# Optimization experiments

Hardware: AMD Instinct MI355X
Metric: run time of the kernel (lower is better)

Reference implementation:

```python
import jax, jax.numpy as jnp
import numpy as np

D_MODEL = 512
NUM_HEADS = 8
D_K = D_MODEL // NUM_HEADS


def setup_inputs() -> dict:
    key = jax.random.key(0)
    kx, kq, kk, kv, ko = jax.random.split(key, 5)
    scale = 1.0 / np.sqrt(D_MODEL)
    return {
        "x": jax.random.normal(kx, (2, 4096, D_MODEL), dtype=jnp.float32),
        "Wq": jax.random.normal(kq, (D_MODEL, D_MODEL), dtype=jnp.float32) * scale,
        "Wk": jax.random.normal(kk, (D_MODEL, D_MODEL), dtype=jnp.float32) * scale,
        "Wv": jax.random.normal(kv, (D_MODEL, D_MODEL), dtype=jnp.float32) * scale,
        "Wo": jax.random.normal(ko, (D_MODEL, D_MODEL), dtype=jnp.float32) * scale,
    }


def reference(x, Wq, Wk, Wv, Wo):
    B, T, D = x.shape
    H, dk = NUM_HEADS, D_K
    # Linear(d,d, bias=False): y = x @ W.T ; weights stored [out,in] like torch
    q = (x @ Wq.T).reshape(B, T, H, dk).transpose(0, 2, 1, 3)  # [B,H,T,dk]
    k = (x @ Wk.T).reshape(B, T, H, dk).transpose(0, 2, 1, 3)
    v = (x @ Wv.T).reshape(B, T, H, dk).transpose(0, 2, 1, 3)
    scores = jnp.einsum("bhqd,bhkd->bhqk", q, k) / np.sqrt(dk)  # [B,H,T,T]
    probs = jax.nn.softmax(scores, axis=-1)
    o = jnp.einsum("bhqk,bhkd->bhqd", probs, v)  # [B,H,T,dk]
    o = o.transpose(0, 2, 1, 3).reshape(B, T, D)
    return o @ Wo.T
```

## Files before the change

### kernel.cpp

```cpp
#include <hip/hip_runtime.h>
#include <hip/hip_bf16.h>

#define SEQ 4096
#define DMODEL 512
#define HEADS 8
#define DK 64
#define BATCH 2
#define MTOT (BATCH * SEQ)
#define NBH (BATCH * HEADS)

typedef __attribute__((ext_vector_type(8))) short bh8;
typedef __attribute__((ext_vector_type(4))) float f4;
typedef __attribute__((ext_vector_type(16))) float f16x;
typedef __attribute__((ext_vector_type(2))) float f2;

union uf { f16x v; f2 h[8]; };

#define MFMA(a, b, c)   __builtin_amdgcn_mfma_f32_16x16x32_bf16(a, b, c, 0, 0, 0)
#define MFMA32(a, b, c) __builtin_amdgcn_mfma_f32_32x32x16_bf16(a, b, c, 0, 0, 0)
#define GLL16(g, l) __builtin_amdgcn_global_load_lds( \
    (const __attribute__((address_space(1))) void*)(g), \
    (__attribute__((address_space(3))) void*)(l), 16, 0, 0)

__device__ __forceinline__ unsigned short f2b(float f) {
    union { float f; unsigned u; } v; v.f = f;
    unsigned r = v.u + 0x7fff + ((v.u >> 16) & 1);
    return (unsigned short)(r >> 16);
}

__device__ __forceinline__ unsigned cvtpk(float lo, float hi) {
    unsigned r;
    asm("v_cvt_pk_bf16_f32 %0, %1, %2" : "=v"(r) : "v"(lo), "v"(hi));
    return r;
}
__device__ __forceinline__ void plswap(unsigned& a, unsigned& b) {
    asm("v_permlane32_swap_b32 %0, %1" : "+v"(a), "+v"(b));
}
__device__ __forceinline__ float wave_max_pair(float x) {
    float b = x; asm("" : "+v"(b));
    float a = x;
    asm("v_permlane32_swap_b32 %0, %1" : "+v"(a), "+v"(b));
    return fmaxf(a, b);
}
__device__ __forceinline__ float wave_sum_pair(float x) {
    float b = x; asm("" : "+v"(b));
    float a = x;
    asm("v_permlane32_swap_b32 %0, %1" : "+v"(a), "+v"(b));
    return a + b;
}
__device__ __forceinline__ f2 pk_add(f2 a, f2 b) {
    f2 d; asm("v_pk_add_f32 %0, %1, %2" : "=v"(d) : "v"(a), "v"(b)); return d;
}
__device__ __forceinline__ f2 pk_mul(f2 a, f2 b) {
    f2 d; asm("v_pk_mul_f32 %0, %1, %2" : "=v"(d) : "v"(a), "v"(b)); return d;
}
__device__ __forceinline__ float max3f(float a, float b, float c) {
    float d; asm("v_max3_f32 %0, %1, %2, %3" : "=v"(d) : "v"(a), "v"(b), "v"(c));
    return d;
}

__global__ __launch_bounds__(256) void convert_k(
    const float* __restrict__ x, const float* __restrict__ wq,
    const float* __restrict__ wk, const float* __restrict__ wv,
    const float* __restrict__ wo, unsigned short* __restrict__ dst)
{
    const size_t i = ((size_t)blockIdx.x * 256 + threadIdx.x) * 4;
    const float* s; size_t o;
    if (i < 4194304u)                 { s = x;  o = i; }
    else if (i < 4194304u + 262144u)  { s = wq; o = i - 4194304u; }
    else if (i < 4194304u + 524288u)  { s = wk; o = i - (4194304u + 262144u); }
    else if (i < 4194304u + 786432u)  { s = wv; o = i - (4194304u + 524288u); }
    else                              { s = wo; o = i - (4194304u + 786432u); }
    float4 v = *(const float4*)(s + o);
    ushort4 u; u.x = f2b(v.x); u.y = f2b(v.y); u.z = f2b(v.z); u.w = f2b(v.w);
    *(ushort4*)(dst + i) = u;
}

__global__ __launch_bounds__(256) void qkv_gemm_mfma(
    const unsigned short* __restrict__ xb,
    const unsigned short* __restrict__ Wb,
    unsigned short* __restrict__ QKV)
{
    const int z = blockIdx.z;
    const unsigned short* A = xb;
    const unsigned short* B = Wb + (size_t)z * (DMODEL * DMODEL);
    const int m0 = blockIdx.x * 128, n0 = blockIdx.y * 128;
    const int tid = threadIdx.x, w = tid >> 6, l = tid & 63;
    const int wr = w >> 1, wc = w & 1;

    __shared__ __align__(16) unsigned short As[128 * 32];
    __shared__ __align__(16) unsigned short Bs[128 * 32];

    f4 acc[4][4] = {};
    const int lrow = l >> 2, lslot = l & 3;

    for (int k0 = 0; k0 < DMODEL; k0 += 32) {
        __syncthreads();
        #pragma unroll
        for (int j = 0; j < 2; ++j) {
            const int row = w * 32 + j * 16 + lrow;
            const int sw = lslot ^ ((row >> 1) & 3);
            GLL16(A + (size_t)(m0 + row) * DMODEL + k0 + sw * 8,
                  (char*)As + (w * 32 + j * 16) * 64);
            GLL16(B + (size_t)(n0 + row) * DMODEL + k0 + sw * 8,
                  (char*)Bs + (w * 32 + j * 16) * 64);
        }
        __syncthreads();
        bh8 af[4], bg[4];
        #pragma unroll
        for (int mi = 0; mi < 4; ++mi) {
            const int r = wr * 64 + mi * 16 + (l & 15);
            af[mi] = *(const bh8*)((const char*)As + r * 64 +
                                   (((l >> 4) * 16) ^ (((r >> 1) & 3) << 4)));
        }
        #pragma unroll
        for (int ni = 0; ni < 4; ++ni) {
            const int r = wc * 64 + ni * 16 + (l & 15);
            bg[ni] = *(const bh8*)((const char*)Bs + r * 64 +
                                   (((l >> 4) * 16) ^ (((r >> 1) & 3) << 4)));
        }
        #pragma unroll
        for (int mi = 0; mi < 4; ++mi)
            #pragma unroll
            for (int ni = 0; ni < 4; ++ni)
                acc[mi][ni] = MFMA(af[mi], bg[ni], acc[mi][ni]);
    }

    unsigned short* Out = QKV + (size_t)z * ((size_t)NBH * SEQ * DK);
    const float sc = (z == 0) ? 0.18033688011112042f : 1.0f;
    #pragma unroll
    for (int mi = 0; mi < 4; ++mi) {
        #pragma unroll
        for (int rg = 0; rg < 4; ++rg) {
            const int m = m0 + wr * 64 + mi * 16 + (l >> 4) * 4 + rg;
            const int b = m >> 12, t = m & (SEQ - 1);
            #pragma unroll
            for (int ni = 0; ni < 4; ++ni) {
                const int n = n0 + wc * 64 + ni * 16 + (l & 15);
                const int h = n >> 6, d = n & 63;
                Out[(((size_t)(b * HEADS + h)) * SEQ + t) * DK + d] =
                    f2b(acc[mi][ni][rg] * sc);
            }
        }
    }
}

__global__ __launch_bounds__(256) void vtrans(
    const unsigned short* __restrict__ Vh, unsigned short* __restrict__ Vt)
{
    const int bh = blockIdx.y, t0 = blockIdx.x * 64;
    __shared__ unsigned short L[64][72];
    const unsigned short* src = Vh + ((size_t)bh * SEQ + t0) * DK;
    const int r = threadIdx.x >> 3, c8 = (threadIdx.x & 7) * 8;
    #pragma unroll
    for (int it = 0; it < 2; ++it) {
        const int row = r + it * 32;
        ushort4 a = *(const ushort4*)(src + (size_t)row * DK + c8);
        ushort4 b = *(const ushort4*)(src + (size_t)row * DK + c8 + 4);
        L[row][c8 + 0] = a.x; L[row][c8 + 1] = a.y; L[row][c8 + 2] = a.z; L[row][c8 + 3] = a.w;
        L[row][c8 + 4] = b.x; L[row][c8 + 5] = b.y; L[row][c8 + 6] = b.z; L[row][c8 + 7] = b.w;
    }
    __syncthreads();
    unsigned short* dst = Vt + (size_t)bh * DK * SEQ + t0;
    #pragma unroll
    for (int it = 0; it < 2; ++it) {
        const int d = r + it * 32;
        ushort4 a, b;
        a.x = L[c8 + 0][d]; a.y = L[c8 + 1][d]; a.z = L[c8 + 2][d]; a.w = L[c8 + 3][d];
        b.x = L[c8 + 4][d]; b.y = L[c8 + 5][d]; b.z = L[c8 + 6][d]; b.w = L[c8 + 7][d];
        *(ushort4*)(dst + (size_t)d * SEQ + c8) = a;
        *(ushort4*)(dst + (size_t)d * SEQ + c8 + 4) = b;
    }
}

__global__ __launch_bounds__(256, 2) void flash_mfma(
    const unsigned short* __restrict__ Qh,
    const unsigned short* __restrict__ Kh,
    const unsigned short* __restrict__ Vtp,
    unsigned short* __restrict__ Ow)
{
    const int bid = blockIdx.x;
    const int bh = bid & 15, q0 = (bid >> 4) * 128;
    const int tid = threadIdx.x, w = tid >> 6, l = tid & 63;
    const int lq = l & 31, hi = l >> 5;

    __shared__ __align__(16) char lds[65536];

    const unsigned short* Qb = Qh + (size_t)bh * SEQ * DK;
    const unsigned short* Kb = Kh + (size_t)bh * SEQ * DK;
    const unsigned short* Vb = Vtp + (size_t)bh * DK * SEQ;

    bh8 qf[4];
    #pragma unroll
    for (int ks = 0; ks < 4; ++ks)
        qf[ks] = *(const bh8*)(Qb + (size_t)(q0 + w * 32 + lq) * DK + ks * 16 + hi * 8);

    int koff[2], voff[2];
    #pragma unroll
    for (int j = 0; j < 2; ++j) {
        const int f = 2 * w + j, rh = f >> 2, ks = f & 3;
        koff[j] = (rh * 32 + lq) * DK + ks * 16 + hi * 8;
        voff[j] = (rh * 32 + lq) * SEQ + ks * 16 + hi * 8;
    }

    f16x oA0 = {}, oA1 = {}, oB0 = {}, oB1 = {};
    float mA = -3.0e38f, lA = 0.f, mB = -3.0e38f, lB = 0.f;

#define STAGE(buf_, half_, kv0_) do {                                         \
    _Pragma("unroll")                                                         \
    for (int j_ = 0; j_ < 2; ++j_) {                                          \
        GLL16(Kb + (size_t)(half_) * (2048 * DK) + (size_t)(kv0_) * DK + koff[j_], \
              lds + (buf_) * 32768 + (half_) * 16384 + (2 * w + j_) * 1024);  \
        GLL16(Vb + (half_) * 2048 + (size_t)(kv0_) + voff[j_],                \
              lds + (buf_) * 32768 + (half_) * 16384 + 8192 + (2 * w + j_) * 1024); \
    }                                                                         \
} while (0)

#define QKT(kb_, sa0_, sa1_) do {                                             \
    __builtin_amdgcn_s_setprio(1);                                            \
    _Pragma("unroll")                                                         \
    for (int ks_ = 0; ks_ < 4; ++ks_) {                                       \
        bh8 k0_ = *(const bh8*)((kb_) + ks_ * 1024);                          \
        bh8 k1_ = *(const bh8*)((kb_) + (4 + ks_) * 1024);                    \
        sa0_ = MFMA32(k0_, qf[ks_], sa0_);                                    \
        sa1_ = MFMA32(k1_, qf[ks_], sa1_);                                    \
    }                                                                         \
    __builtin_amdgcn_s_setprio(0);                                            \
} while (0)

#define SMPV(vb_, sa0_, sa1_, m_run_, l_run_, o0_, o1_) do {                  \
    float a_ = fmaxf(sa0_[0], sa0_[1]);                                       \
    float b_ = fmaxf(sa1_[0], sa1_[1]);                                       \
    _Pragma("unroll")                                                         \
    for (int r_ = 2; r_ < 16; r_ += 2) {                                      \
        a_ = max3f(a_, sa0_[r_], sa0_[r_ + 1]);                               \
        b_ = max3f(b_, sa1_[r_], sa1_[r_ + 1]);                               \
    }                                                                         \
    const float mx_ = wave_max_pair(fmaxf(a_, b_));                           \
    const bool skip_ = __all(mx_ <= m_run_ + 8.0f);                           \
    float mnew_ = m_run_, corr_ = 1.0f;                                       \
    if (!skip_) {                                                             \
        mnew_ = fmaxf(m_run_, mx_);                                           \
        corr_ = __builtin_amdgcn_exp2f(m_run_ - mnew_);                       \
    }                                                                         \
    uf U0_, U1_; U0_.v = sa0_; U1_.v = sa1_;                                  \
    f2 nm2_; nm2_[0] = -mnew_; nm2_[1] = -mnew_;                              \
    f2 p2_[16];                                                               \
    _Pragma("unroll")                                                         \
    for (int i_ = 0; i_ < 8; ++i_) {                                          \
        f2 t0_ = pk_add(U0_.h[i_], nm2_);                                     \
        f2 t1_ = pk_add(U1_.h[i_], nm2_);                                     \
        f2 e0_, e1_;                                                          \
        e0_[0] = __builtin_amdgcn_exp2f(t0_[0]);                              \
        e0_[1] = __builtin_amdgcn_exp2f(t0_[1]);                              \
        e1_[0] = __builtin_amdgcn_exp2f(t1_[0]);                              \
        e1_[1] = __builtin_amdgcn_exp2f(t1_[1]);                              \
        p2_[i_] = e0_; p2_[8 + i_] = e1_;                                     \
    }                                                                         \
    f2 s0_ = pk_add(p2_[0], p2_[1]),   s1_ = pk_add(p2_[2], p2_[3]);          \
    f2 s2_ = pk_add(p2_[4], p2_[5]),   s3_ = pk_add(p2_[6], p2_[7]);          \
    f2 s4_ = pk_add(p2_[8], p2_[9]),   s5_ = pk_add(p2_[10], p2_[11]);        \
    f2 s6_ = pk_add(p2_[12], p2_[13]), s7_ = pk_add(p2_[14], p2_[15]);        \
    s0_ = pk_add(s0_, s1_); s2_ = pk_add(s2_, s3_);                           \
    s4_ = pk_add(s4_, s5_); s6_ = pk_add(s6_, s7_);                           \
    s0_ = pk_add(s0_, s2_); s4_ = pk_add(s4_, s6_);                           \
    s0_ = pk_add(s0_, s4_);                                                   \
    const float psum_ = wave_sum_pair(s0_[0] + s0_[1]);                       \
    if (!skip_) {                                                             \
        m_run_ = mnew_;                                                       \
        l_run_ = l_run_ * corr_ + psum_;                                      \
        f2 c2_; c2_[0] = corr_; c2_[1] = corr_;                               \
        uf O0_, O1_; O0_.v = o0_; O1_.v = o1_;                                \
        _Pragma("unroll")                                                     \
        for (int i_ = 0; i_ < 8; ++i_) {                                      \
            O0_.h[i_] = pk_mul(O0_.h[i_], c2_);                               \
            O1_.h[i_] = pk_mul(O1_.h[i_], c2_);                               \
        }                                                                     \
        o0_ = O0_.v; o1_ = O1_.v;                                             \
    } else {                                                                  \
        l_run_ += psum_;                                                      \
    }                                                                         \
    bh8 pf_[4];                                                               \
    _Pragma("unroll")                                                         \
    for (int cb_ = 0; cb_ < 2; ++cb_) {                                       \
        unsigned k0_ = cvtpk(p2_[8 * cb_ + 0][0], p2_[8 * cb_ + 0][1]);       \
        unsigned k1_ = cvtpk(p2_[8 * cb_ + 1][0], p2_[8 * cb_ + 1][1]);       \
        unsigned k2_ = cvtpk(p2_[8 * cb_ + 2][0], p2_[8 * cb_ + 2][1]);       \
        unsigned k3_ = cvtpk(p2_[8 * cb_ + 3][0], p2_[8 * cb_ + 3][1]);       \
        unsigned k4_ = cvtpk(p2_[8 * cb_ + 4][0], p2_[8 * cb_ + 4][1]);       \
        unsigned k5_ = cvtpk(p2_[8 * cb_ + 5][0], p2_[8 * cb_ + 5][1]);       \
        unsigned k6_ = cvtpk(p2_[8 * cb_ + 6][0], p2_[8 * cb_ + 6][1]);       \
        unsigned k7_ = cvtpk(p2_[8 * cb_ + 7][0], p2_[8 * cb_ + 7][1]);       \
        plswap(k0_, k2_); plswap(k1_, k3_); plswap(k4_, k6_); plswap(k5_, k7_);\
        union { unsigned u[4]; bh8 v; } f0_, f1_;                             \
        f0_.u[0] = k0_; f0_.u[1] = k1_; f0_.u[2] = k2_; f0_.u[3] = k3_;       \
        f1_.u[0] = k4_; f1_.u[1] = k5_; f1_.u[2] = k6_; f1_.u[3] = k7_;       \
        pf_[cb_ * 2 + 0] = f0_.v;                                             \
        pf_[cb_ * 2 + 1] = f1_.v;                                             \
    }                                                                         \
    __builtin_amdgcn_s_setprio(1);                                            \
    _Pragma("unroll")                                                         \
    for (int ks_ = 0; ks_ < 4; ++ks_) {                                       \
        bh8 v0_ = *(const bh8*)((vb_) + ks_ * 1024);                          \
        bh8 v1_ = *(const bh8*)((vb_) + (4 + ks_) * 1024);                    \
        o0_ = MFMA32(v0_, pf_[ks_], o0_);                                     \
        o1_ = MFMA32(v1_, pf_[ks_], o1_);                                     \
    }                                                                         \
    __builtin_amdgcn_s_setprio(0);                                            \
} while (0)

    STAGE(0, 0, 0);
    STAGE(0, 1, 0);
    __syncthreads();
    int cur = 0;
    const char* myfrag = lds + l * 16;

    for (int t = 0; t < 32; ++t) {
        if (t < 31) {
            STAGE(cur ^ 1, 0, (t + 1) * 64);
            STAGE(cur ^ 1, 1, (t + 1) * 64);
        }

        const char* kbA = myfrag + cur * 32768;
        const char* kbB = kbA + 16384;

        f16x sA0 = {}, sA1 = {}, sB0 = {}, sB1 = {};
        QKT(kbA, sA0, sA1);
        QKT(kbB, sB0, sB1);
        SMPV(kbA + 8192, sA0, sA1, mA, lA, oA0, oA1);
        SMPV(kbB + 8192, sB0, sB1, mB, lB, oB0, oB1);

        __syncthreads();
        cur ^= 1;
    }
#undef STAGE
#undef QKT
#undef SMPV

    const float mt = fmaxf(mA, mB);
    const float cA = __builtin_amdgcn_exp2f(mA - mt);
    const float cB = __builtin_amdgcn_exp2f(mB - mt);
    f16x o0, o1;
    #pragma unroll
    for (int r = 0; r < 16; ++r) {
        o0[r] = oA0[r] * cA + oB0[r] * cB;
        o1[r] = oA1[r] * cA + oB1[r] * cB;
    }
    const float inv = 1.0f / (lA * cA + lB * cB);

    char* Tb = lds + w * 4096;
    #pragma unroll
    for (int db = 0; db < 2; ++db) {
        f16x ov = db ? o1 : o0;
        #pragma unroll
        for (int j = 0; j < 8; ++j) {
            const int r = 2 * j;
            const int d = db * 32 + (r & 3) + 8 * (r >> 2) + 4 * hi;
            unsigned pk = cvtpk(ov[r] * inv, ov[r + 1] * inv);
            *(unsigned*)(Tb + lq * 128 + ((d * 2) ^ ((lq & 7) << 4))) = pk;
        }
    }
    __syncthreads();
    const int b = bh >> 3, h = bh & 7;
    const int row = l >> 1, half = l & 1;
    const int q = q0 + w * 32 + row;
    unsigned short* dst = Ow + ((size_t)b * SEQ + q) * DMODEL + h * DK + half * 32;
    #pragma unroll
    for (int i = 0; i < 4; ++i) {
        const int byte = (half * 64 + i * 16) ^ ((row & 7) << 4);
        uint4 vv = *(const uint4*)(Tb + row * 128 + byte);
        *(uint4*)(dst + i * 8) = vv;
    }
}

__global__ __launch_bounds__(256) void out_gemm_mfma(
    const unsigned short* __restrict__ Ob,
    const unsigned short* __restrict__ Wob,
    float* __restrict__ out)
{
    const int m0 = blockIdx.x * 128, n0 = blockIdx.y * 128;
    const int tid = threadIdx.x, w = tid >> 6, l = tid & 63;
    const int wr = w >> 1, wc = w & 1;

    __shared__ __align__(16) unsigned short As[128 * 32];
    __shared__ __align__(16) unsigned short Bs[128 * 32];

    f4 acc[4][4] = {};
    const int lrow = l >> 2, lslot = l & 3;

    for (int k0 = 0; k0 < DMODEL; k0 += 32) {
        __syncthreads();
        #pragma unroll
        for (int j = 0; j < 2; ++j) {
            const int row = w * 32 + j * 16 + lrow;
            const int sw = lslot ^ ((row >> 1) & 3);
            GLL16(Ob + (size_t)(m0 + row) * DMODEL + k0 + sw * 8,
                  (char*)As + (w * 32 + j * 16) * 64);
            GLL16(Wob + (size_t)(n0 + row) * DMODEL + k0 + sw * 8,
                  (char*)Bs + (w * 32 + j * 16) * 64);
        }
        __syncthreads();
        bh8 af[4], bg[4];
        #pragma unroll
        for (int mi = 0; mi < 4; ++mi) {
            const int r = wr * 64 + mi * 16 + (l & 15);
            af[mi] = *(const bh8*)((const char*)As + r * 64 +
                                   (((l >> 4) * 16) ^ (((r >> 1) & 3) << 4)));
        }
        #pragma unroll
        for (int ni = 0; ni < 4; ++ni) {
            const int r = wc * 64 + ni * 16 + (l & 15);
            bg[ni] = *(const bh8*)((const char*)Bs + r * 64 +
                                   (((l >> 4) * 16) ^ (((r >> 1) & 3) << 4)));
        }
        #pragma unroll
        for (int mi = 0; mi < 4; ++mi)
            #pragma unroll
            for (int ni = 0; ni < 4; ++ni)
                acc[mi][ni] = MFMA(af[mi], bg[ni], acc[mi][ni]);
    }

    #pragma unroll
    for (int mi = 0; mi < 4; ++mi) {
        #pragma unroll
        for (int rg = 0; rg < 4; ++rg) {
            const int m = m0 + wr * 64 + mi * 16 + (l >> 4) * 4 + rg;
            #pragma unroll
            for (int ni = 0; ni < 4; ++ni) {
                const int n = n0 + wc * 64 + ni * 16 + (l & 15);
                out[(size_t)m * DMODEL + n] = acc[mi][ni][rg];
            }
        }
    }
}

extern "C" void kernel_launch(void* const* d_in, const int* in_sizes, int n_in,
                              void* d_out, int out_size, void* d_ws, size_t ws_size,
                              hipStream_t stream)
{
    const float* x  = (const float*)d_in[0];
    const float* Wq = (const float*)d_in[1];
    const float* Wk = (const float*)d_in[2];
    const float* Wv = (const float*)d_in[3];
    const float* Wo = (const float*)d_in[4];
    float* out = (float*)d_out;

    unsigned short* ws = (unsigned short*)d_ws;
    unsigned short* xb  = ws;
    unsigned short* Wb  = xb + 4194304;
    unsigned short* QKV = Wb + 4 * 262144;
    unsigned short* Vt  = QKV + 3 * 4194304;
    unsigned short* Ow  = Vt + 4194304;
    unsigned short* Qh = QKV;
    unsigned short* Kh = QKV + 4194304;
    unsigned short* Vh = QKV + 2 * 4194304;

    convert_k<<<5120, 256, 0, stream>>>(x, Wq, Wk, Wv, Wo, ws);
    qkv_gemm_mfma<<<dim3(MTOT / 128, DMODEL / 128, 3), 256, 0, stream>>>(xb, Wb, QKV);
    vtrans<<<dim3(SEQ / 64, NBH), 256, 0, stream>>>(Vh, Vt);
    flash_mfma<<<512, 256, 0, stream>>>(Qh, Kh, Vt, Ow);
    out_gemm_mfma<<<dim3(MTOT / 128, DMODEL / 128), 256, 0, stream>>>(
        Ow, Wb + 3 * 262144, out);
}
```

Baseline: 141.0 us.

## Software-pipeline PV MFMA one tile behind softmax with register-held V

The PV matrix multiply for each KV tile is deferred to the next loop iteration. V fragments are preloaded into registers, and the packed probabilities are kept across iterations, so the MFMAs for tile t-1 can issue next to the softmax VALU work for tile t. A final PV step after the loop drains the pipeline. The change raises live register count (V and P fragments for both halves), which risks lower occupancy or spills.

```diff
diff --git a/kernel.cpp b/kernel.cpp
--- a/kernel.cpp
+++ b/kernel.cpp
@@ -205,6 +205,8 @@
 
     f16x oA0 = {}, oA1 = {}, oB0 = {}, oB1 = {};
     float mA = -3.0e38f, lA = 0.f, mB = -3.0e38f, lB = 0.f;
+    bh8 vA[8], vB[8];
+    bh8 pfA[4], pfB[4];
 
 #define STAGE(buf_, half_, kv0_) do {                                         \
     _Pragma("unroll")                                                         \
@@ -228,7 +230,23 @@
     __builtin_amdgcn_s_setprio(0);                                            \
 } while (0)
 
-#define SMPV(vb_, sa0_, sa1_, m_run_, l_run_, o0_, o1_) do {                  \
+#define VLOADR(vb_, vr_) do {                                                 \
+    _Pragma("unroll")                                                         \
+    for (int k_ = 0; k_ < 8; ++k_)                                            \
+        (vr_)[k_] = *(const bh8*)((vb_) + k_ * 1024);                         \
+} while (0)
+
+#define PVREG(vr_, pf_, o0_, o1_) do {                                        \
+    __builtin_amdgcn_s_setprio(1);                                            \
+    _Pragma("unroll")                                                         \
+    for (int ks_ = 0; ks_ < 4; ++ks_) {                                       \
+        o0_ = MFMA32((vr_)[ks_],     (pf_)[ks_], o0_);                        \
+        o1_ = MFMA32((vr_)[4 + ks_], (pf_)[ks_], o1_);                        \
+    }                                                                         \
+    __builtin_amdgcn_s_setprio(0);                                            \
+} while (0)
+
+#define SM_PACK(sa0_, sa1_, m_run_, l_run_, o0_, o1_, pf_) do {               \
     float a_ = fmaxf(sa0_[0], sa0_[1]);                                       \
     float b_ = fmaxf(sa1_[0], sa1_[1]);                                       \
     _Pragma("unroll")                                                         \
@@ -280,7 +298,6 @@
     } else {                                                                  \
         l_run_ += psum_;                                                      \
     }                                                                         \
-    bh8 pf_[4];                                                               \
     _Pragma("unroll")                                                         \
     for (int cb_ = 0; cb_ < 2; ++cb_) {                                       \
         unsigned k0_ = cvtpk(p2_[8 * cb_ + 0][0], p2_[8 * cb_ + 0][1]);       \
@@ -295,18 +312,9 @@
         union { unsigned u[4]; bh8 v; } f0_, f1_;                             \
         f0_.u[0] = k0_; f0_.u[1] = k1_; f0_.u[2] = k2_; f0_.u[3] = k3_;       \
         f1_.u[0] = k4_; f1_.u[1] = k5_; f1_.u[2] = k6_; f1_.u[3] = k7_;       \
-        pf_[cb_ * 2 + 0] = f0_.v;                                             \
-        pf_[cb_ * 2 + 1] = f1_.v;                                             \
-    }                                                                         \
-    __builtin_amdgcn_s_setprio(1);                                            \
-    _Pragma("unroll")                                                         \
-    for (int ks_ = 0; ks_ < 4; ++ks_) {                                       \
-        bh8 v0_ = *(const bh8*)((vb_) + ks_ * 1024);                          \
-        bh8 v1_ = *(const bh8*)((vb_) + (4 + ks_) * 1024);                    \
-        o0_ = MFMA32(v0_, pf_[ks_], o0_);                                     \
-        o1_ = MFMA32(v1_, pf_[ks_], o1_);                                     \
-    }                                                                         \
-    __builtin_amdgcn_s_setprio(0);                                            \
+        (pf_)[cb_ * 2 + 0] = f0_.v;                                           \
+        (pf_)[cb_ * 2 + 1] = f1_.v;                                           \
+    }                                                                         \
 } while (0)
 
     STAGE(0, 0, 0);
@@ -327,15 +335,28 @@
         f16x sA0 = {}, sA1 = {}, sB0 = {}, sB1 = {};
         QKT(kbA, sA0, sA1);
         QKT(kbB, sB0, sB1);
-        SMPV(kbA + 8192, sA0, sA1, mA, lA, oA0, oA1);
-        SMPV(kbB + 8192, sB0, sB1, mB, lB, oB0, oB1);
+
+        if (t > 0) {
+            PVREG(vA, pfA, oA0, oA1);
+            PVREG(vB, pfB, oB0, oB1);
+        }
+
+        VLOADR(kbA + 8192, vA);
+        VLOADR(kbB + 8192, vB);
+
+        SM_PACK(sA0, sA1, mA, lA, oA0, oA1, pfA);
+        SM_PACK(sB0, sB1, mB, lB, oB0, oB1, pfB);
 
         __syncthreads();
         cur ^= 1;
     }
+    PVREG(vA, pfA, oA0, oA1);
+    PVREG(vB, pfB, oB0, oB1);
 #undef STAGE
 #undef QKT
-#undef SMPV
+#undef VLOADR
+#undef PVREG
+#undef SM_PACK
 
     const float mt = fmaxf(mA, mB);
     const float cA = __builtin_amdgcn_exp2f(mA - mt);
```

Measured after the change: 185.8 us. 31.8% more time.

## Split KV sequence across two blocks per query tile and merge partials

Applied to the files above, without the earlier changes.

Each query tile's attention is now split into two KV halves handled by separate blocks, doubling the grid to 1024 blocks. Each block processes 32 keys per sub-tile instead of 64, which halves LDS use and raises launch bounds to allow four blocks per CU. Each block writes unnormalized bf16 partial outputs plus per-row max and sum. A new merge kernel rescales and combines the two halves into the output layout. The cost is an extra launch, extra global traffic for the partials, bf16 rounding of the unnormalized partials, and reuse of workspace buffers for scratch.

```diff
diff --git a/kernel.cpp b/kernel.cpp
--- a/kernel.cpp
+++ b/kernel.cpp
@@ -26,6 +26,12 @@
     union { float f; unsigned u; } v; v.f = f;
     unsigned r = v.u + 0x7fff + ((v.u >> 16) & 1);
     return (unsigned short)(r >> 16);
+}
+__device__ __forceinline__ float lo2f(unsigned u) {
+    union { unsigned u; float f; } v; v.u = u << 16; return v.f;
+}
+__device__ __forceinline__ float hi2f(unsigned u) {
+    union { unsigned u; float f; } v; v.u = u & 0xffff0000u; return v.f;
 }
 
 __device__ __forceinline__ unsigned cvtpk(float lo, float hi) {
@@ -173,18 +179,22 @@
     }
 }
 
-__global__ __launch_bounds__(256, 2) void flash_mfma(
+__global__ __launch_bounds__(256, 4) void flash_mfma(
     const unsigned short* __restrict__ Qh,
     const unsigned short* __restrict__ Kh,
     const unsigned short* __restrict__ Vtp,
-    unsigned short* __restrict__ Ow)
+    unsigned short* __restrict__ P0,
+    unsigned short* __restrict__ P1,
+    float* __restrict__ MLp)
 {
     const int bid = blockIdx.x;
-    const int bh = bid & 15, q0 = (bid >> 4) * 128;
+    const int bh = bid & 15, qt = (bid >> 4) & 31, kvp = bid >> 9;
+    const int q0 = qt * 128;
     const int tid = threadIdx.x, w = tid >> 6, l = tid & 63;
     const int lq = l & 31, hi = l >> 5;
-
-    __shared__ __align__(16) char lds[65536];
+    const int kvbase = kvp * 2048;
+
+    __shared__ __align__(16) char lds[32768];
 
     const unsigned short* Qb = Qh + (size_t)bh * SEQ * DK;
     const unsigned short* Kb = Kh + (size_t)bh * SEQ * DK;
@@ -195,12 +205,20 @@
     for (int ks = 0; ks < 4; ++ks)
         qf[ks] = *(const bh8*)(Qb + (size_t)(q0 + w * 32 + lq) * DK + ks * 16 + hi * 8);
 
-    int koff[2], voff[2];
+    int srcoff[2], dstoff[2], isK[2];
     #pragma unroll
     for (int j = 0; j < 2; ++j) {
-        const int f = 2 * w + j, rh = f >> 2, ks = f & 3;
-        koff[j] = (rh * 32 + lq) * DK + ks * 16 + hi * 8;
-        voff[j] = (rh * 32 + lq) * SEQ + ks * 16 + hi * 8;
+        const int f = 2 * w + j;
+        if (f < 4) {
+            isK[j] = 1;
+            srcoff[j] = lq * DK + f * 16 + hi * 8;
+            dstoff[j] = f * 1024;
+        } else {
+            isK[j] = 0;
+            const int dt = (f - 4) >> 1, ks = (f - 4) & 1;
+            srcoff[j] = (dt * 32 + lq) * SEQ + ks * 16 + hi * 8;
+            dstoff[j] = 4096 + (f - 4) * 1024;
+        }
     }
 
     f16x oA0 = {}, oA1 = {}, oB0 = {}, oB1 = {};
@@ -209,32 +227,29 @@
 #define STAGE(buf_, half_, kv0_) do {                                         \
     _Pragma("unroll")                                                         \
     for (int j_ = 0; j_ < 2; ++j_) {                                          \
-        GLL16(Kb + (size_t)(half_) * (2048 * DK) + (size_t)(kv0_) * DK + koff[j_], \
-              lds + (buf_) * 32768 + (half_) * 16384 + (2 * w + j_) * 1024);  \
-        GLL16(Vb + (half_) * 2048 + (size_t)(kv0_) + voff[j_],                \
-              lds + (buf_) * 32768 + (half_) * 16384 + 8192 + (2 * w + j_) * 1024); \
+        char* d_ = lds + (buf_) * 16384 + (half_) * 8192 + dstoff[j_];        \
+        if (isK[j_])                                                          \
+            GLL16(Kb + (size_t)(kvbase + (half_) * 1024 + (kv0_)) * DK + srcoff[j_], d_); \
+        else                                                                  \
+            GLL16(Vb + (size_t)(kvbase + (half_) * 1024 + (kv0_)) + srcoff[j_], d_); \
     }                                                                         \
 } while (0)
 
-#define QKT(kb_, sa0_, sa1_) do {                                             \
+#define QKT(kb_, sa_) do {                                                    \
     __builtin_amdgcn_s_setprio(1);                                            \
     _Pragma("unroll")                                                         \
-    for (int ks_ = 0; ks_ < 4; ++ks_) {                                       \
-        bh8 k0_ = *(const bh8*)((kb_) + ks_ * 1024);                          \
-        bh8 k1_ = *(const bh8*)((kb_) + (4 + ks_) * 1024);                    \
-        sa0_ = MFMA32(k0_, qf[ks_], sa0_);                                    \
-        sa1_ = MFMA32(k1_, qf[ks_], sa1_);                                    \
-    }                                                                         \
+    for (int ks_ = 0; ks_ < 4; ++ks_)                                         \
+        sa_ = MFMA32(*(const bh8*)((kb_) + ks_ * 1024), qf[ks_], sa_);        \
     __builtin_amdgcn_s_setprio(0);                                            \
 } while (0)
 
-#define SMPV(vb_, sa0_, sa1_, m_run_, l_run_, o0_, o1_) do {                  \
-    float a_ = fmaxf(sa0_[0], sa0_[1]);                                       \
-    float b_ = fmaxf(sa1_[0], sa1_[1]);                                       \
+#define SMPV(kb_, sa_, m_run_, l_run_, o0_, o1_) do {                         \
+    float a_ = fmaxf(sa_[0], sa_[1]);                                         \
+    float b_ = fmaxf(sa_[2], sa_[3]);                                         \
     _Pragma("unroll")                                                         \
-    for (int r_ = 2; r_ < 16; r_ += 2) {                                      \
-        a_ = max3f(a_, sa0_[r_], sa0_[r_ + 1]);                               \
-        b_ = max3f(b_, sa1_[r_], sa1_[r_ + 1]);                               \
+    for (int r_ = 4; r_ < 16; r_ += 4) {                                      \
+        a_ = max3f(a_, sa_[r_], sa_[r_ + 1]);                                 \
+        b_ = max3f(b_, sa_[r_ + 2], sa_[r_ + 3]);                             \
     }                                                                         \
     const float mx_ = wave_max_pair(fmaxf(a_, b_));                           \
     const bool skip_ = __all(mx_ <= m_run_ + 8.0f);                           \
@@ -243,28 +258,20 @@
         mnew_ = fmaxf(m_run_, mx_);                                           \
         corr_ = __builtin_amdgcn_exp2f(m_run_ - mnew_);                       \
     }                                                                         \
-    uf U0_, U1_; U0_.v = sa0_; U1_.v = sa1_;                                  \
+    uf U_; U_.v = sa_;                                                        \
     f2 nm2_; nm2_[0] = -mnew_; nm2_[1] = -mnew_;                              \
-    f2 p2_[16];                                                               \
+    f2 p2_[8];                                                                \
     _Pragma("unroll")                                                         \
     for (int i_ = 0; i_ < 8; ++i_) {                                          \
-        f2 t0_ = pk_add(U0_.h[i_], nm2_);                                     \
-        f2 t1_ = pk_add(U1_.h[i_], nm2_);                                     \
-        f2 e0_, e1_;                                                          \
-        e0_[0] = __builtin_amdgcn_exp2f(t0_[0]);                              \
-        e0_[1] = __builtin_amdgcn_exp2f(t0_[1]);                              \
-        e1_[0] = __builtin_amdgcn_exp2f(t1_[0]);                              \
-        e1_[1] = __builtin_amdgcn_exp2f(t1_[1]);                              \
-        p2_[i_] = e0_; p2_[8 + i_] = e1_;                                     \
+        f2 t_ = pk_add(U_.h[i_], nm2_);                                       \
+        f2 e_;                                                                \
+        e_[0] = __builtin_amdgcn_exp2f(t_[0]);                                \
+        e_[1] = __builtin_amdgcn_exp2f(t_[1]);                                \
+        p2_[i_] = e_;                                                         \
     }                                                                         \
-    f2 s0_ = pk_add(p2_[0], p2_[1]),   s1_ = pk_add(p2_[2], p2_[3]);          \
-    f2 s2_ = pk_add(p2_[4], p2_[5]),   s3_ = pk_add(p2_[6], p2_[7]);          \
-    f2 s4_ = pk_add(p2_[8], p2_[9]),   s5_ = pk_add(p2_[10], p2_[11]);        \
-    f2 s6_ = pk_add(p2_[12], p2_[13]), s7_ = pk_add(p2_[14], p2_[15]);        \
-    s0_ = pk_add(s0_, s1_); s2_ = pk_add(s2_, s3_);                           \
-    s4_ = pk_add(s4_, s5_); s6_ = pk_add(s6_, s7_);                           \
-    s0_ = pk_add(s0_, s2_); s4_ = pk_add(s4_, s6_);                           \
-    s0_ = pk_add(s0_, s4_);                                                   \
+    f2 s0_ = pk_add(p2_[0], p2_[1]), s1_ = pk_add(p2_[2], p2_[3]);            \
+    f2 s2_ = pk_add(p2_[4], p2_[5]), s3_ = pk_add(p2_[6], p2_[7]);            \
+    s0_ = pk_add(s0_, s1_); s2_ = pk_add(s2_, s3_); s0_ = pk_add(s0_, s2_);   \
     const float psum_ = wave_sum_pair(s0_[0] + s0_[1]);                       \
     if (!skip_) {                                                             \
         m_run_ = mnew_;                                                       \
@@ -280,58 +287,46 @@
     } else {                                                                  \
         l_run_ += psum_;                                                      \
     }                                                                         \
-    bh8 pf_[4];                                                               \
-    _Pragma("unroll")                                                         \
-    for (int cb_ = 0; cb_ < 2; ++cb_) {                                       \
-        unsigned k0_ = cvtpk(p2_[8 * cb_ + 0][0], p2_[8 * cb_ + 0][1]);       \
-        unsigned k1_ = cvtpk(p2_[8 * cb_ + 1][0], p2_[8 * cb_ + 1][1]);       \
-        unsigned k2_ = cvtpk(p2_[8 * cb_ + 2][0], p2_[8 * cb_ + 2][1]);       \
-        unsigned k3_ = cvtpk(p2_[8 * cb_ + 3][0], p2_[8 * cb_ + 3][1]);       \
-        unsigned k4_ = cvtpk(p2_[8 * cb_ + 4][0], p2_[8 * cb_ + 4][1]);       \
-        unsigned k5_ = cvtpk(p2_[8 * cb_ + 5][0], p2_[8 * cb_ + 5][1]);       \
-        unsigned k6_ = cvtpk(p2_[8 * cb_ + 6][0], p2_[8 * cb_ + 6][1]);       \
-        unsigned k7_ = cvtpk(p2_[8 * cb_ + 7][0], p2_[8 * cb_ + 7][1]);       \
-        plswap(k0_, k2_); plswap(k1_, k3_); plswap(k4_, k6_); plswap(k5_, k7_);\
-        union { unsigned u[4]; bh8 v; } f0_, f1_;                             \
-        f0_.u[0] = k0_; f0_.u[1] = k1_; f0_.u[2] = k2_; f0_.u[3] = k3_;       \
-        f1_.u[0] = k4_; f1_.u[1] = k5_; f1_.u[2] = k6_; f1_.u[3] = k7_;       \
-        pf_[cb_ * 2 + 0] = f0_.v;                                             \
-        pf_[cb_ * 2 + 1] = f1_.v;                                             \
-    }                                                                         \
+    unsigned k0_ = cvtpk(p2_[0][0], p2_[0][1]);                               \
+    unsigned k1_ = cvtpk(p2_[1][0], p2_[1][1]);                               \
+    unsigned k2_ = cvtpk(p2_[2][0], p2_[2][1]);                               \
+    unsigned k3_ = cvtpk(p2_[3][0], p2_[3][1]);                               \
+    unsigned k4_ = cvtpk(p2_[4][0], p2_[4][1]);                               \
+    unsigned k5_ = cvtpk(p2_[5][0], p2_[5][1]);                               \
+    unsigned k6_ = cvtpk(p2_[6][0], p2_[6][1]);                               \
+    unsigned k7_ = cvtpk(p2_[7][0], p2_[7][1]);                               \
+    plswap(k0_, k2_); plswap(k1_, k3_); plswap(k4_, k6_); plswap(k5_, k7_);   \
+    union { unsigned u[4]; bh8 v; } f0_, f1_;                                 \
+    f0_.u[0] = k0_; f0_.u[1] = k1_; f0_.u[2] = k2_; f0_.u[3] = k3_;           \
+    f1_.u[0] = k4_; f1_.u[1] = k5_; f1_.u[2] = k6_; f1_.u[3] = k7_;           \
+    const char* vb_ = (kb_) + 4096;                                           \
     __builtin_amdgcn_s_setprio(1);                                            \
-    _Pragma("unroll")                                                         \
-    for (int ks_ = 0; ks_ < 4; ++ks_) {                                       \
-        bh8 v0_ = *(const bh8*)((vb_) + ks_ * 1024);                          \
-        bh8 v1_ = *(const bh8*)((vb_) + (4 + ks_) * 1024);                    \
-        o0_ = MFMA32(v0_, pf_[ks_], o0_);                                     \
-        o1_ = MFMA32(v1_, pf_[ks_], o1_);                                     \
-    }                                                                         \
+    o0_ = MFMA32(*(const bh8*)(vb_ + 0),    f0_.v, o0_);                      \
+    o0_ = MFMA32(*(const bh8*)(vb_ + 1024), f1_.v, o0_);                      \
+    o1_ = MFMA32(*(const bh8*)(vb_ + 2048), f0_.v, o1_);                      \
+    o1_ = MFMA32(*(const bh8*)(vb_ + 3072), f1_.v, o1_);                      \
     __builtin_amdgcn_s_setprio(0);                                            \
 } while (0)
 
     STAGE(0, 0, 0);
     STAGE(0, 1, 0);
     __syncthreads();
-    int cur = 0;
     const char* myfrag = lds + l * 16;
 
     for (int t = 0; t < 32; ++t) {
         if (t < 31) {
-            STAGE(cur ^ 1, 0, (t + 1) * 64);
-            STAGE(cur ^ 1, 1, (t + 1) * 64);
-        }
-
-        const char* kbA = myfrag + cur * 32768;
-        const char* kbB = kbA + 16384;
-
-        f16x sA0 = {}, sA1 = {}, sB0 = {}, sB1 = {};
-        QKT(kbA, sA0, sA1);
-        QKT(kbB, sB0, sB1);
-        SMPV(kbA + 8192, sA0, sA1, mA, lA, oA0, oA1);
-        SMPV(kbB + 8192, sB0, sB1, mB, lB, oB0, oB1);
+            STAGE((t + 1) & 1, 0, (t + 1) * 32);
+            STAGE((t + 1) & 1, 1, (t + 1) * 32);
+        }
+
+        const char* base = myfrag + (t & 1) * 16384;
+        f16x sA = {}, sB = {};
+        QKT(base, sA);
+        QKT(base + 8192, sB);
+        SMPV(base, sA, mA, lA, oA0, oA1);
+        SMPV(base + 8192, sB, mB, lB, oB0, oB1);
 
         __syncthreads();
-        cur ^= 1;
     }
 #undef STAGE
 #undef QKT
@@ -346,7 +341,7 @@
         o0[r] = oA0[r] * cA + oB0[r] * cB;
         o1[r] = oA1[r] * cA + oB1[r] * cB;
     }
-    const float inv = 1.0f / (lA * cA + lB * cB);
+    const float l_tot = lA * cA + lB * cB;
 
     char* Tb = lds + w * 4096;
     #pragma unroll
@@ -356,20 +351,69 @@
         for (int j = 0; j < 8; ++j) {
             const int r = 2 * j;
             const int d = db * 32 + (r & 3) + 8 * (r >> 2) + 4 * hi;
-            unsigned pk = cvtpk(ov[r] * inv, ov[r + 1] * inv);
+            unsigned pk = cvtpk(ov[r], ov[r + 1]);
             *(unsigned*)(Tb + lq * 128 + ((d * 2) ^ ((lq & 7) << 4))) = pk;
         }
     }
     __syncthreads();
-    const int b = bh >> 3, h = bh & 7;
+    unsigned short* po = kvp ? P1 : P0;
     const int row = l >> 1, half = l & 1;
-    const int q = q0 + w * 32 + row;
-    unsigned short* dst = Ow + ((size_t)b * SEQ + q) * DMODEL + h * DK + half * 32;
+    const int qloc = w * 32 + row;
+    unsigned short* dst = po + (((size_t)bh * 32 + qt) * 128 + qloc) * 64 + half * 32;
     #pragma unroll
     for (int i = 0; i < 4; ++i) {
         const int byte = (half * 64 + i * 16) ^ ((row & 7) << 4);
-        uint4 vv = *(const uint4*)(Tb + row * 128 + byte);
-        *(uint4*)(dst + i * 8) = vv;
+        *(uint4*)(dst + i * 8) = *(const uint4*)(Tb + row * 128 + byte);
+    }
+    if (hi == 0) {
+        float* mlb = MLp + (((size_t)kvp * 16 + bh) * 32 + qt) * 256;
+        mlb[w * 32 + lq] = mt;
+        mlb[128 + w * 32 + lq] = l_tot;
+    }
+}
+
+__global__ __launch_bounds__(256) void merge_k(
+    const unsigned short* __restrict__ P0,
+    const unsigned short* __restrict__ P1,
+    const float* __restrict__ MLp,
+    unsigned short* __restrict__ Ow)
+{
+    const int qt = blockIdx.x, bh = blockIdx.y;
+    const int tid = threadIdx.x;
+    __shared__ float C0[128], C1[128];
+    if (tid < 128) {
+        const float* m0b = MLp + (((size_t)bh) * 32 + qt) * 256;
+        const float* m1b = MLp + (((size_t)16 + bh) * 32 + qt) * 256;
+        const float m0 = m0b[tid], l0 = m0b[128 + tid];
+        const float m1 = m1b[tid], l1 = m1b[128 + tid];
+        const float m = fmaxf(m0, m1);
+        const float c0 = __builtin_amdgcn_exp2f(m0 - m);
+        const float c1 = __builtin_amdgcn_exp2f(m1 - m);
+        const float inv = 1.0f / (l0 * c0 + l1 * c1);
+        C0[tid] = c0 * inv;
+        C1[tid] = c1 * inv;
+    }
+    __syncthreads();
+    const int q = tid >> 1, half = tid & 1;
+    const float c0 = C0[q], c1 = C1[q];
+    const size_t off = (((size_t)bh * 32 + qt) * 128 + q) * 64 + half * 32;
+    const int b = bh >> 3, h = bh & 7;
+    unsigned short* dst = Ow + ((size_t)b * SEQ + qt * 128 + q) * DMODEL + h * DK + half * 32;
+    #pragma unroll
+    for (int i = 0; i < 4; ++i) {
+        uint4 a = *(const uint4*)(P0 + off + i * 8);
+        uint4 bb = *(const uint4*)(P1 + off + i * 8);
+        uint4 o;
+        unsigned* ap = (unsigned*)&a;
+        unsigned* bp = (unsigned*)&bb;
+        unsigned* op = (unsigned*)&o;
+        #pragma unroll
+        for (int k = 0; k < 4; ++k) {
+            const unsigned ua = ap[k], ub = bp[k];
+            op[k] = cvtpk(lo2f(ua) * c0 + lo2f(ub) * c1,
+                          hi2f(ua) * c0 + hi2f(ub) * c1);
+        }
+        *(uint4*)(dst + i * 8) = o;
     }
 }
 
@@ -455,10 +499,15 @@
     unsigned short* Kh = QKV + 4194304;
     unsigned short* Vh = QKV + 2 * 4194304;
 
+    unsigned short* P0 = xb;
+    unsigned short* P1 = Vh;
+    float* MLp = (float*)Wb;
+
     convert_k<<<5120, 256, 0, stream>>>(x, Wq, Wk, Wv, Wo, ws);
     qkv_gemm_mfma<<<dim3(MTOT / 128, DMODEL / 128, 3), 256, 0, stream>>>(xb, Wb, QKV);
     vtrans<<<dim3(SEQ / 64, NBH), 256, 0, stream>>>(Vh, Vt);
-    flash_mfma<<<512, 256, 0, stream>>>(Qh, Kh, Vt, Ow);
+    flash_mfma<<<1024, 256, 0, stream>>>(Qh, Kh, Vt, P0, P1, MLp);
+    merge_k<<<dim3(32, 16), 256, 0, stream>>>(P0, P1, MLp, Ow);
     out_gemm_mfma<<<dim3(MTOT / 128, DMODEL / 128), 256, 0, stream>>>(
         Ow, Wb + 3 * 262144, out);
 }
```

New measurement: 336.1 us. +138.3%, slower.

## Double flash attention block to 8 waves covering 256 queries per block

Applied to the files above, without the earlier changes.

The flash kernel now launches 256 blocks of 512 threads, each handling 256 query rows, so every staged K/V tile in LDS is shared by eight waves instead of four. Each wave issues one async global-to-LDS load per half-tile instead of two, which halves per-wave load work and the number of K/V loads from global memory. The cost is a larger barrier group per iteration and only 256 blocks across the device, which may leave some compute units underused or unbalanced.

```diff
diff --git a/kernel.cpp b/kernel.cpp
--- a/kernel.cpp
+++ b/kernel.cpp
@@ -173,14 +173,14 @@
     }
 }
 
-__global__ __launch_bounds__(256, 2) void flash_mfma(
+__global__ __launch_bounds__(512, 2) void flash_mfma(
     const unsigned short* __restrict__ Qh,
     const unsigned short* __restrict__ Kh,
     const unsigned short* __restrict__ Vtp,
     unsigned short* __restrict__ Ow)
 {
     const int bid = blockIdx.x;
-    const int bh = bid & 15, q0 = (bid >> 4) * 128;
+    const int bh = bid & 15, q0 = (bid >> 4) * 256;
     const int tid = threadIdx.x, w = tid >> 6, l = tid & 63;
     const int lq = l & 31, hi = l >> 5;
 
@@ -195,25 +195,17 @@
     for (int ks = 0; ks < 4; ++ks)
         qf[ks] = *(const bh8*)(Qb + (size_t)(q0 + w * 32 + lq) * DK + ks * 16 + hi * 8);
 
-    int koff[2], voff[2];
-    #pragma unroll
-    for (int j = 0; j < 2; ++j) {
-        const int f = 2 * w + j, rh = f >> 2, ks = f & 3;
-        koff[j] = (rh * 32 + lq) * DK + ks * 16 + hi * 8;
-        voff[j] = (rh * 32 + lq) * SEQ + ks * 16 + hi * 8;
-    }
+    const int koff = ((w >> 2) * 32 + lq) * DK + (w & 3) * 16 + hi * 8;
+    const int voff = ((w >> 2) * 32 + lq) * SEQ + (w & 3) * 16 + hi * 8;
 
     f16x oA0 = {}, oA1 = {}, oB0 = {}, oB1 = {};
     float mA = -3.0e38f, lA = 0.f, mB = -3.0e38f, lB = 0.f;
 
 #define STAGE(buf_, half_, kv0_) do {                                         \
-    _Pragma("unroll")                                                         \
-    for (int j_ = 0; j_ < 2; ++j_) {                                          \
-        GLL16(Kb + (size_t)(half_) * (2048 * DK) + (size_t)(kv0_) * DK + koff[j_], \
-              lds + (buf_) * 32768 + (half_) * 16384 + (2 * w + j_) * 1024);  \
-        GLL16(Vb + (half_) * 2048 + (size_t)(kv0_) + voff[j_],                \
-              lds + (buf_) * 32768 + (half_) * 16384 + 8192 + (2 * w + j_) * 1024); \
-    }                                                                         \
+    GLL16(Kb + (size_t)(half_) * (2048 * DK) + (size_t)(kv0_) * DK + koff,    \
+          lds + (buf_) * 32768 + (half_) * 16384 + w * 1024);                 \
+    GLL16(Vb + (half_) * 2048 + (size_t)(kv0_) + voff,                        \
+          lds + (buf_) * 32768 + (half_) * 16384 + 8192 + w * 1024);          \
 } while (0)
 
 #define QKT(kb_, sa0_, sa1_) do {                                             \
@@ -228,7 +220,7 @@
     __builtin_amdgcn_s_setprio(0);                                            \
 } while (0)
 
-#define SMPV(vb_, sa0_, sa1_, m_run_, l_run_, o0_, o1_) do {                  \
+#define SMPV(kb_, sa0_, sa1_, m_run_, l_run_, o0_, o1_) do {                  \
     float a_ = fmaxf(sa0_[0], sa0_[1]);                                       \
     float b_ = fmaxf(sa1_[0], sa1_[1]);                                       \
     _Pragma("unroll")                                                         \
@@ -298,11 +290,12 @@
         pf_[cb_ * 2 + 0] = f0_.v;                                             \
         pf_[cb_ * 2 + 1] = f1_.v;                                             \
     }                                                                         \
+    const char* vb_ = (kb_) + 8192;                                           \
     __builtin_amdgcn_s_setprio(1);                                            \
     _Pragma("unroll")                                                         \
     for (int ks_ = 0; ks_ < 4; ++ks_) {                                       \
-        bh8 v0_ = *(const bh8*)((vb_) + ks_ * 1024);                          \
-        bh8 v1_ = *(const bh8*)((vb_) + (4 + ks_) * 1024);                    \
+        bh8 v0_ = *(const bh8*)(vb_ + ks_ * 1024);                            \
+        bh8 v1_ = *(const bh8*)(vb_ + (4 + ks_) * 1024);                      \
         o0_ = MFMA32(v0_, pf_[ks_], o0_);                                     \
         o1_ = MFMA32(v1_, pf_[ks_], o1_);                                     \
     }                                                                         \
@@ -327,8 +320,8 @@
         f16x sA0 = {}, sA1 = {}, sB0 = {}, sB1 = {};
         QKT(kbA, sA0, sA1);
         QKT(kbB, sB0, sB1);
-        SMPV(kbA + 8192, sA0, sA1, mA, lA, oA0, oA1);
-        SMPV(kbB + 8192, sB0, sB1, mB, lB, oB0, oB1);
+        SMPV(kbA, sA0, sA1, mA, lA, oA0, oA1);
+        SMPV(kbB, sB0, sB1, mB, lB, oB0, oB1);
 
         __syncthreads();
         cur ^= 1;
@@ -458,7 +451,7 @@
     convert_k<<<5120, 256, 0, stream>>>(x, Wq, Wk, Wv, Wo, ws);
     qkv_gemm_mfma<<<dim3(MTOT / 128, DMODEL / 128, 3), 256, 0, stream>>>(xb, Wb, QKV);
     vtrans<<<dim3(SEQ / 64, NBH), 256, 0, stream>>>(Vh, Vt);
-    flash_mfma<<<512, 256, 0, stream>>>(Qh, Kh, Vt, Ow);
+    flash_mfma<<<256, 512, 0, stream>>>(Qh, Kh, Vt, Ow);
     out_gemm_mfma<<<dim3(MTOT / 128, DMODEL / 128), 256, 0, stream>>>(
         Ow, Wb + 3 * 262144, out);
 }
```

After: 134.2 us, median of 2. 1.05x faster.
